# Performance work log

Measured on AMD Instinct MI355X. Metric: run time of the kernel, lower is better.

Reference implementation:

```python
import jax, jax.numpy as jnp
import numpy as np

N1, N2, N3 = 3, 5, 7
BATCH = 262144


def setup_inputs() -> dict:
    key = jax.random.key(0)
    k1, k2, k3, k4 = jax.random.split(key, 4)
    D1 = jax.random.normal(k1, (BATCH, N1, N1), dtype=jnp.float32)
    D2 = jax.random.normal(k2, (BATCH, N2, N2), dtype=jnp.float32)
    D3 = jax.random.normal(k3, (BATCH, N3, N3), dtype=jnp.float32)
    # learned Clebsch-Gordan coefficient tensor (the layer's only weight)
    cg_coeffs = jax.random.normal(k4, (N1, N2, N3), dtype=jnp.float32)
    return {"D1": D1, "D2": D2, "D3": D3, "cg_coeffs": cg_coeffs}


def reference(D1, D2, D3, cg_coeffs):
    # lhs: rotate cg by D1 (left) and D2 (middle) -> [x, n1, n2, n3]
    lhs = jnp.einsum('xai,xbj,ijc->xabc', D1, D2, cg_coeffs)
    # rhs: rotate cg by D3 on the last index -> [x, n1, n2, n3]
    rhs = jnp.einsum('abi,xic->xabc', cg_coeffs, D3)
    residual = lhs - rhs
    return jnp.mean(residual * residual)
```

## Files before the change

### kernel.cpp

```cpp
#include <hip/hip_runtime.h>

#define TPB 256

__global__ __launch_bounds__(TPB, 3) void cg_main_kernel(
    const float* __restrict__ D1, const float* __restrict__ D2,
    const float* __restrict__ D3, const float* __restrict__ cg,
    float* __restrict__ partials)
{
    __shared__ __align__(16) float s_d3[TPB * 49];

    const int tid = threadIdx.x;
    const int blk = blockIdx.x;

    {
        const float4* g = (const float4*)(D3 + (size_t)blk * (TPB * 49));
        float4* s = (float4*)s_d3;
        #pragma unroll
        for (int k = 0; k < 13; ++k) {
            int i = k * TPB + tid;
            if (i < TPB * 49 / 4) s[i] = g[i];
        }
    }

    float d1[9], d2[25];
    {
        const float* p1 = D1 + (size_t)(blk * TPB + tid) * 9;
        #pragma unroll
        for (int i = 0; i < 9; ++i) d1[i] = p1[i];
        const float* p2 = D2 + (size_t)(blk * TPB + tid) * 25;
        #pragma unroll
        for (int j = 0; j < 25; ++j) d2[j] = p2[j];
    }
    __syncthreads();

    float acc = 0.0f;
    #pragma unroll
    for (int c = 0; c < 7; ++c) {
        float d3c[7];
        #pragma unroll
        for (int i = 0; i < 7; ++i) d3c[i] = s_d3[tid * 49 + i * 7 + c];

        #pragma unroll
        for (int a = 0; a < 3; ++a) {
            float U[5];
            #pragma unroll
            for (int j = 0; j < 5; ++j)
                U[j] = fmaf(d1[a * 3 + 2], cg[70 + j * 7 + c],
                       fmaf(d1[a * 3 + 1], cg[35 + j * 7 + c],
                            d1[a * 3 + 0] * cg[      j * 7 + c]));
            #pragma unroll
            for (int b = 0; b < 5; ++b) {
                float L = d2[b * 5] * U[0];
                #pragma unroll
                for (int j = 1; j < 5; ++j) L = fmaf(d2[b * 5 + j], U[j], L);
                float R = cg[(a * 5 + b) * 7] * d3c[0];
                #pragma unroll
                for (int i = 1; i < 7; ++i) R = fmaf(cg[(a * 5 + b) * 7 + i], d3c[i], R);
                const float r = L - R;
                acc = fmaf(r, r, acc);
            }
        }
    }

    #pragma unroll
    for (int off = 32; off > 0; off >>= 1)
        acc += __shfl_down(acc, off, 64);
    __shared__ float wsum[TPB / 64];
    if ((tid & 63) == 0) wsum[tid >> 6] = acc;
    __syncthreads();
    if (tid == 0) {
        float s = 0.0f;
        #pragma unroll
        for (int w = 0; w < TPB / 64; ++w) s += wsum[w];
        partials[blk] = s;
    }
}

__global__ __launch_bounds__(256) void cg_reduce_kernel(
    const float* __restrict__ partials, float* __restrict__ out,
    int n, float inv)
{
    const int tid = threadIdx.x;
    float s = 0.0f;
    for (int i = tid; i < n; i += 256) s += partials[i];
    #pragma unroll
    for (int off = 32; off > 0; off >>= 1)
        s += __shfl_down(s, off, 64);
    __shared__ float wsum[4];
    if ((tid & 63) == 0) wsum[tid >> 6] = s;
    __syncthreads();
    if (tid == 0) {
        float t = 0.0f;
        #pragma unroll
        for (int w = 0; w < 4; ++w) t += wsum[w];
        out[0] = t * inv;
    }
}

extern "C" void kernel_launch(void* const* d_in, const int* in_sizes, int n_in,
                              void* d_out, int out_size, void* d_ws, size_t ws_size,
                              hipStream_t stream)
{
    const float* D1 = (const float*)d_in[0];
    const float* D2 = (const float*)d_in[1];
    const float* D3 = (const float*)d_in[2];
    const float* cg = (const float*)d_in[3];
    float* out      = (float*)d_out;
    float* partials = (float*)d_ws;

    const int batch   = in_sizes[0] / 9;
    const int nblocks = batch / TPB;
    const float inv   = 1.0f / ((float)batch * 105.0f);

    cg_main_kernel<<<nblocks, TPB, 0, stream>>>(D1, D2, D3, cg, partials);
    cg_reduce_kernel<<<1, 256, 0, stream>>>(partials, out, nblocks, inv);
}
```

Baseline: 27.51 us.

## Split each batch element across two lanes with per-wave persistent chunk loop

```diff
diff --git a/kernel.cpp b/kernel.cpp
--- a/kernel.cpp
+++ b/kernel.cpp
@@ -1,63 +1,96 @@
 #include <hip/hip_runtime.h>
 
-#define TPB 256
+#define CHUNK 32
+#define NCHUNK 8192
+#define SLICE_F 2476
+#define NBLOCKS 1024
+#define NWAVES (NBLOCKS * 4)
 
-__global__ __launch_bounds__(TPB, 3) void cg_main_kernel(
+__global__ __launch_bounds__(256, 4) void cg_main_kernel(
     const float* __restrict__ D1, const float* __restrict__ D2,
     const float* __restrict__ D3, const float* __restrict__ cg,
     float* __restrict__ partials)
 {
-    __shared__ __align__(16) float s_d3[TPB * 49];
+    __shared__ __align__(16) float s_all[4][SLICE_F];
 
     const int tid = threadIdx.x;
-    const int blk = blockIdx.x;
+    const int wv  = tid >> 6;
+    const int l   = tid & 63;
+    const int le  = l & 31;
+    const int sub = l >> 5;
 
-    {
-        const float4* g = (const float4*)(D3 + (size_t)blk * (TPB * 49));
-        float4* s = (float4*)s_d3;
-        #pragma unroll
-        for (int k = 0; k < 13; ++k) {
-            int i = k * TPB + tid;
-            if (i < TPB * 49 / 4) s[i] = g[i];
-        }
+    float* sl  = s_all[wv];
+    float* s2  = sl;
+    float* s3  = sl + 800;
+    float* scg = sl + 2368;
+
+    #pragma unroll
+    for (int k = 0; k < 2; ++k) {
+        int i = k * 64 + l;
+        if (i < 105) scg[i] = cg[i];
     }
 
-    float d1[9], d2[25];
-    {
-        const float* p1 = D1 + (size_t)(blk * TPB + tid) * 9;
+    const int gw = blockIdx.x * 4 + wv;
+    float acc = 0.0f;
+
+    for (int ch = gw; ch < NCHUNK; ch += NWAVES) {
+        {
+            const float4* g2 = (const float4*)(D2 + (size_t)ch * 800);
+            float4* t2 = (float4*)s2;
+            #pragma unroll
+            for (int k = 0; k < 4; ++k) { int i = k * 64 + l; if (i < 200) t2[i] = g2[i]; }
+            const float4* g3 = (const float4*)(D3 + (size_t)ch * 1568);
+            float4* t3 = (float4*)s3;
+            #pragma unroll
+            for (int k = 0; k < 7; ++k) { int i = k * 64 + l; if (i < 392) t3[i] = g3[i]; }
+        }
+
+        const int e = ch * CHUNK + le;
+        float d1[9];
+        {
+            const float* p1 = D1 + (size_t)e * 9;
+            #pragma unroll
+            for (int i = 0; i < 9; ++i) d1[i] = p1[i];
+        }
+
+        float d2r[25];
         #pragma unroll
-        for (int i = 0; i < 9; ++i) d1[i] = p1[i];
-        const float* p2 = D2 + (size_t)(blk * TPB + tid) * 25;
-        #pragma unroll
-        for (int j = 0; j < 25; ++j) d2[j] = p2[j];
-    }
-    __syncthreads();
-
-    float acc = 0.0f;
-    #pragma unroll
-    for (int c = 0; c < 7; ++c) {
-        float d3c[7];
-        #pragma unroll
-        for (int i = 0; i < 7; ++i) d3c[i] = s_d3[tid * 49 + i * 7 + c];
+        for (int j = 0; j < 25; ++j) d2r[j] = s2[le * 25 + j];
 
         #pragma unroll
-        for (int a = 0; a < 3; ++a) {
-            float U[5];
-            #pragma unroll
-            for (int j = 0; j < 5; ++j)
-                U[j] = fmaf(d1[a * 3 + 2], cg[70 + j * 7 + c],
-                       fmaf(d1[a * 3 + 1], cg[35 + j * 7 + c],
-                            d1[a * 3 + 0] * cg[      j * 7 + c]));
-            #pragma unroll
-            for (int b = 0; b < 5; ++b) {
-                float L = d2[b * 5] * U[0];
+        for (int t = 0; t < 4; ++t) {
+            const int c = sub * 4 + t;
+            if (c < 7) {
+                float cgv[15];
                 #pragma unroll
-                for (int j = 1; j < 5; ++j) L = fmaf(d2[b * 5 + j], U[j], L);
-                float R = cg[(a * 5 + b) * 7] * d3c[0];
+                for (int i = 0; i < 3; ++i)
+                    #pragma unroll
+                    for (int j = 0; j < 5; ++j)
+                        cgv[i * 5 + j] = scg[i * 35 + j * 7 + c];
+                float d3c[7];
                 #pragma unroll
-                for (int i = 1; i < 7; ++i) R = fmaf(cg[(a * 5 + b) * 7 + i], d3c[i], R);
-                const float r = L - R;
-                acc = fmaf(r, r, acc);
+                for (int i = 0; i < 7; ++i) d3c[i] = s3[le * 49 + i * 7 + c];
+
+                #pragma unroll
+                for (int a = 0; a < 3; ++a) {
+                    float U[5];
+                    #pragma unroll
+                    for (int j = 0; j < 5; ++j)
+                        U[j] = fmaf(d1[a * 3 + 2], cgv[10 + j],
+                               fmaf(d1[a * 3 + 1], cgv[5 + j],
+                                    d1[a * 3 + 0] * cgv[j]));
+                    #pragma unroll
+                    for (int b = 0; b < 5; ++b) {
+                        float L = d2r[b * 5] * U[0];
+                        #pragma unroll
+                        for (int j = 1; j < 5; ++j) L = fmaf(d2r[b * 5 + j], U[j], L);
+                        float R = cg[(a * 5 + b) * 7] * d3c[0];
+                        #pragma unroll
+                        for (int i = 1; i < 7; ++i) R = fmaf(cg[(a * 5 + b) * 7 + i], d3c[i], R);
+                        const float r = L - R;
+                        acc = fmaf(r, r, acc);
+                    }
+                }
             }
         }
     }
@@ -65,15 +98,7 @@
     #pragma unroll
     for (int off = 32; off > 0; off >>= 1)
         acc += __shfl_down(acc, off, 64);
-    __shared__ float wsum[TPB / 64];
-    if ((tid & 63) == 0) wsum[tid >> 6] = acc;
-    __syncthreads();
-    if (tid == 0) {
-        float s = 0.0f;
-        #pragma unroll
-        for (int w = 0; w < TPB / 64; ++w) s += wsum[w];
-        partials[blk] = s;
-    }
+    if (l == 0) partials[gw] = acc;
 }
 
 __global__ __launch_bounds__(256) void cg_reduce_kernel(
@@ -108,10 +133,9 @@
     float* out      = (float*)d_out;
     float* partials = (float*)d_ws;
 
-    const int batch   = in_sizes[0] / 9;
-    const int nblocks = batch / TPB;
-    const float inv   = 1.0f / ((float)batch * 105.0f);
+    const int batch = in_sizes[0] / 9;
+    const float inv = 1.0f / ((float)batch * 105.0f);
 
-    cg_main_kernel<<<nblocks, TPB, 0, stream>>>(D1, D2, D3, cg, partials);
-    cg_reduce_kernel<<<1, 256, 0, stream>>>(partials, out, nblocks, inv);
+    cg_main_kernel<<<NBLOCKS, 256, 0, stream>>>(D1, D2, D3, cg, partials);
+    cg_reduce_kernel<<<1, 256, 0, stream>>>(partials, out, NWAVES, inv);
 }
```

Result: slower. 40.15 us (+45.9%).
